# Performance work log

Measured on AMD Instinct MI355X. Metric: run time of the kernel, lower is better.

## Reference

```python
import jax, jax.numpy as jnp
import numpy as np

EPS = 1e-8  # torch.nn.CosineSimilarity default eps


def _cosine_sim(a, b):
    # cosine similarity along channel dim (axis=1), matching torch semantics:
    # dot / (max(||a||, eps) * max(||b||, eps))
    na = jnp.maximum(jnp.sqrt(jnp.sum(a * a, axis=1)), EPS)
    nb = jnp.maximum(jnp.sqrt(jnp.sum(b * b, axis=1)), EPS)
    return jnp.sum(a * b, axis=1) / (na * nb)  # [B, T]


def setup_inputs() -> dict:
    key = jax.random.key(0)
    k1, k2, k3 = jax.random.split(key, 3)
    B, C, T, O, K = 8, 512, 4096, 512, 3
    feature = jax.random.normal(k1, (B, C, T), dtype=jnp.float32)
    embedding = jax.random.normal(k2, (B, C, T), dtype=jnp.float32)
    weight = jax.random.normal(k3, (O, C, K), dtype=jnp.float32) * 0.05
    return {"feature": feature, "embedding": embedding, "weight": weight}


def reference(feature, embedding, weight):
    B, C, T = feature.shape
    O = weight.shape[0]
    K = 3  # kernel_size is structurally 3 in this module

    # shifted embeddings with zero padding (left / right neighbors)
    emb_l = jnp.pad(embedding[:, :, :-1], ((0, 0), (0, 0), (1, 0)))
    emb_r = jnp.pad(embedding[:, :, 1:], ((0, 0), (0, 0), (0, 1)))
    sim = jnp.stack(
        [_cosine_sim(embedding, emb_l),
         _cosine_sim(embedding, embedding),
         _cosine_sim(embedding, emb_r)],
        axis=1,
    )  # [B, 3, T]

    # tile: first C rows = sim_l, next C = sim_c, last C = sim_r -> [B, 3C, T]
    att = jnp.repeat(sim, C, axis=1)

    # im2col (nn.Unfold with kernel (3,1), padding (1,0)): channel-major layout
    f_pad = jnp.pad(feature, ((0, 0), (0, 0), (1, 1)))  # [B, C, T+2]
    inp_unf = jnp.stack([f_pad[:, :, k:k + T] for k in range(K)], axis=2)
    inp_unf = inp_unf.reshape(B, C * K, T)  # row index = c*3 + k (torch unfold order)

    w_flat = weight.reshape(O, C * K)
    # out[b,o,t] = sum_i (inp_unf * att)[b,i,t] * w_flat[o,i]
    out = jnp.einsum('bit,oi->bot', inp_unf * att, w_flat)
    return out
```

## Files before the change

kernel.cpp:

```cpp
#include <hip/hip_runtime.h>
#include <hip/hip_bf16.h>
#include <stdint.h>

#define B_ 8
#define C_ 512
#define T_ 4096
#define O_ 512
#define KP_ 1728
#define EPS_ 1e-8f

#define BM 128
#define BN 128
#define FTP_ROWS 4104

typedef unsigned short ushort_t;
typedef __attribute__((ext_vector_type(4))) float f32x4;
typedef __attribute__((ext_vector_type(8))) short bf16x8;

__device__ __forceinline__ ushort_t f2bf(float f) {
  union { float f; uint32_t u; } x; x.f = f;
  uint32_t u = x.u;
  uint32_t r = (u + 0x7FFFu + ((u >> 16) & 1u)) >> 16;
  return (ushort_t)r;
}

#define GLOAD16(gsrc, ldst) \
  __builtin_amdgcn_global_load_lds((const __attribute__((address_space(1))) unsigned int*)(gsrc), \
                                   (__attribute__((address_space(3))) unsigned int*)(ldst), 16, 0, 0)

__global__ void sim_reduce_kernel(const float* __restrict__ emb,
                                  float* __restrict__ nn_out,
                                  float* __restrict__ dl_out) {
  const int b = blockIdx.y;
  const int t0 = (blockIdx.x * 64 + threadIdx.x) * 4;
  const int cty = threadIdx.y;
  float nn0=0.f,nn1=0.f,nn2=0.f,nn3=0.f;
  float dl0=0.f,dl1=0.f,dl2=0.f,dl3=0.f;
  const float* base = emb + (size_t)b * C_ * T_;
  for (int c = cty * 128; c < cty * 128 + 128; ++c) {
    const float* row = base + (size_t)c * T_;
    float4 v = *(const float4*)(row + t0);
    float el = (t0 > 0) ? row[t0 - 1] : 0.f;
    nn0 += v.x*v.x; nn1 += v.y*v.y; nn2 += v.z*v.z; nn3 += v.w*v.w;
    dl0 += v.x*el;  dl1 += v.y*v.x; dl2 += v.z*v.y; dl3 += v.w*v.z;
  }
  __shared__ float red[4][64*8];
  float* myr = &red[cty][threadIdx.x * 8];
  if (cty != 0) {
    myr[0]=nn0; myr[1]=nn1; myr[2]=nn2; myr[3]=nn3;
    myr[4]=dl0; myr[5]=dl1; myr[6]=dl2; myr[7]=dl3;
  }
  __syncthreads();
  if (cty == 0) {
    for (int q = 1; q < 4; ++q) {
      float* r = &red[q][threadIdx.x * 8];
      nn0+=r[0]; nn1+=r[1]; nn2+=r[2]; nn3+=r[3];
      dl0+=r[4]; dl1+=r[5]; dl2+=r[6]; dl3+=r[7];
    }
    float* nb = nn_out + (size_t)b * T_ + t0;
    float* db = dl_out + (size_t)b * T_ + t0;
    nb[0]=nn0; nb[1]=nn1; nb[2]=nn2; nb[3]=nn3;
    db[0]=dl0; db[1]=dl1; db[2]=dl2; db[3]=dl3;
  }
}

__global__ void prep_small_kernel(const float* __restrict__ nn,
                                  const float* __restrict__ dl,
                                  float* __restrict__ rat,
                                  const float* __restrict__ w,
                                  ushort_t* __restrict__ wbf) {
  const int bid = blockIdx.x;
  if (bid < 128) {
    const int idx = bid * 256 + threadIdx.x;
    const int b = idx >> 12;
    const int t = idx & (T_ - 1);
    const float* nnb = nn + (size_t)b * T_;
    const float* dlb = dl + (size_t)b * T_;
    float nncur = nnb[t];
    float ncur = fmaxf(sqrtf(nncur), EPS_);
    float sc = nncur / (ncur * ncur);
    float sl = 0.f, sr = 0.f;
    if (t > 0) {
      float np = fmaxf(sqrtf(nnb[t - 1]), EPS_);
      sl = dlb[t] / (ncur * np);
    }
    if (t < T_ - 1) {
      float nx = fmaxf(sqrtf(nnb[t + 1]), EPS_);
      sr = dlb[t + 1] / (ncur * nx);
    }
    float shr = (fabsf(sr) < 1e-6f) ? copysignf(1e-6f, sr) : sr;
    float shc = fmaxf(sc, 1e-6f);
    float* ratb = rat + (size_t)b * T_;
    ratb[t] = sl / shr;
    ratb[(size_t)B_ * T_ + t] = shr / shc;
    ratb[(size_t)2 * B_ * T_ + t] = sc;
  } else {
    const int idx = (bid - 128) * 256 + threadIdx.x;
    if (idx >= O_ * KP_) return;
    const int o = idx / KP_;
    const int p = idx - o * KP_;
    const int g = p / 576; const int r = p - g * 576;
    const int k = r / 192; const int j = r - k * 192;
    const int c_lo = (512 * g - k + 2) / 3;
    const int c_hi = (512 * g + 511 - k) / 3;
    const int c = (c_lo & ~7) + j;
    float v = (c >= c_lo && c <= c_hi) ? w[((size_t)o * C_ + c) * 3 + k] : 0.f;
    wbf[idx] = f2bf(v);
  }
}

__global__ void transpose_kernel(const float* __restrict__ feat, ushort_t* __restrict__ Ftp) {
  const int b = blockIdx.z;
  const int c0 = blockIdx.y * 64;
  const int tid = threadIdx.x;
  if (blockIdx.x == T_ / 64) {
    if (tid < 64)        Ftp[((size_t)b * FTP_ROWS + 0) * 512 + c0 + tid] = 0;
    else if (tid < 128)  Ftp[((size_t)b * FTP_ROWS + T_ + 1) * 512 + c0 + (tid - 64)] = 0;
    return;
  }
  const int t0 = blockIdx.x * 64;
  __shared__ ushort_t LT[64 * 72];
  {
    const int cl = tid >> 2;
    const int tq = (tid & 3) * 16;
    const float* src = feat + ((size_t)b * C_ + c0 + cl) * T_ + t0 + tq;
    for (int q = 0; q < 4; ++q) {
      float4 v = *(const float4*)(src + q * 4);
      const int t = tq + q * 4;
      LT[(t + 0) * 72 + cl] = f2bf(v.x);
      LT[(t + 1) * 72 + cl] = f2bf(v.y);
      LT[(t + 2) * 72 + cl] = f2bf(v.z);
      LT[(t + 3) * 72 + cl] = f2bf(v.w);
    }
  }
  __syncthreads();
  {
    const int tl = tid >> 2;
    const int cq = (tid & 3) * 16;
    ushort_t* dst = Ftp + ((size_t)b * FTP_ROWS + t0 + tl + 1) * 512 + c0 + cq;
    *(uint4*)(dst) = *(const uint4*)&LT[tl * 72 + cq];
    *(uint4*)(dst + 8) = *(const uint4*)&LT[tl * 72 + cq + 8];
  }
}

__global__ __launch_bounds__(256, 3)
void conv_gemm_kernel(const ushort_t* __restrict__ Ftp,
                      const ushort_t* __restrict__ wbf,
                      const float* __restrict__ rat,
                      float* __restrict__ out) {
  __shared__ __align__(16) ushort_t Al[BM * 64];
  __shared__ __align__(16) ushort_t Bl[BN * 64];

  const int b = blockIdx.z;
  const int oBase = blockIdx.y * BM;
  const int tBase = blockIdx.x * BN;

  const int tid = threadIdx.x;
  const int lane = tid & 63;
  const int wid = tid >> 6;
  const int wm = wid >> 1;
  const int wn = wid & 1;
  const int llo = lane & 15, lhi = lane >> 4;

  const int r8 = lane >> 3;
  const int chs = ((lane & 7) ^ r8) * 8;

  const ushort_t* aS = wbf + (size_t)(oBase + wid * 32 + r8) * KP_ + chs;
  const ushort_t* bS = Ftp + ((size_t)b * FTP_ROWS + tBase + wid * 32 + r8) * 512 + chs;

  ushort_t* aD = &Al[(wid * 32) * 64 + lane * 8];
  ushort_t* bD = &Bl[(wid * 32) * 64 + lane * 8];

  const int fra = (wm * 64 + llo) * 64 + ((lhi ^ (llo & 7)) * 8);
  const int frb = (wn * 64 + llo) * 64 + ((lhi ^ (llo & 7)) * 8);

  const float* ratB = rat + (size_t)b * T_ + tBase + wn * 64 + llo;

  f32x4 acc[4][4];
  const f32x4 vzero = {0.f, 0.f, 0.f, 0.f};
#pragma unroll
  for (int m = 0; m < 4; ++m)
#pragma unroll
    for (int n = 0; n < 4; ++n) acc[m][n] = vzero;

#pragma unroll
  for (int u = 0; u < 27; ++u) {
    const int s2 = (u < 9) ? u : ((u < 18) ? u + 9 : u - 9);
    const int g = s2 / 9, rr = s2 - g * 9, k = rr / 3, jb = rr - k * 3;
    const int c_st = ((512 * g - k + 2) / 3) & ~7;
    const int boff = k * 512 + c_st + jb * 64;

    __syncthreads();
#pragma unroll
    for (int i = 0; i < 4; ++i) {
      GLOAD16(aS + (size_t)(i * 8) * KP_ + s2 * 64, aD + i * 512);
      GLOAD16(bS + (size_t)(i * 8) * 512 + boff,    bD + i * 512);
    }
    __syncthreads();

#pragma unroll
    for (int h = 0; h < 2; ++h) {
      bf16x8 af[4], bfv[4];
#pragma unroll
      for (int m = 0; m < 4; ++m)
        af[m] = *(const bf16x8*)&Al[(fra ^ (h * 32)) + m * 1024];
#pragma unroll
      for (int n = 0; n < 4; ++n)
        bfv[n] = *(const bf16x8*)&Bl[(frb ^ (h * 32)) + n * 1024];
#pragma unroll
      for (int m = 0; m < 4; ++m)
#pragma unroll
        for (int n = 0; n < 4; ++n)
          acc[m][n] = __builtin_amdgcn_mfma_f32_16x16x32_bf16(af[m], bfv[n], acc[m][n], 0, 0, 0);
    }

    if (u == 8 || u == 17 || u == 26) {
      const int sel = (u == 8) ? 0 : (u == 17) ? 1 : 2;
#pragma unroll
      for (int n = 0; n < 4; ++n) {
        const float s = ratB[(size_t)sel * B_ * T_ + n * 16];
#pragma unroll
        for (int m = 0; m < 4; ++m) acc[m][n] *= s;
      }
    }
  }

  float* outB = out + ((size_t)b * O_ + oBase) * T_ + tBase;
#pragma unroll
  for (int m = 0; m < 4; ++m) {
    const int r0 = wm * 64 + m * 16 + lhi * 4;
#pragma unroll
    for (int n = 0; n < 4; ++n) {
      const int cg = wn * 64 + n * 16 + llo;
#pragma unroll
      for (int r = 0; r < 4; ++r)
        outB[(size_t)(r0 + r) * T_ + cg] = acc[m][n][r];
    }
  }
}

extern "C" void kernel_launch(void* const* d_in, const int* in_sizes, int n_in,
                              void* d_out, int out_size, void* d_ws, size_t ws_size,
                              hipStream_t stream) {
  const float* feature   = (const float*)d_in[0];
  const float* embedding = (const float*)d_in[1];
  const float* weight    = (const float*)d_in[2];
  float* out = (float*)d_out;

  float* ws  = (float*)d_ws;
  float* nn  = ws;
  float* dl  = nn + (size_t)B_ * T_;
  float* rat = dl + (size_t)B_ * T_;
  ushort_t* wbf = (ushort_t*)(rat + (size_t)3 * B_ * T_);
  ushort_t* Ftp = wbf + (size_t)O_ * KP_;

  sim_reduce_kernel<<<dim3(T_ / 256, B_), dim3(64, 4), 0, stream>>>(embedding, nn, dl);
  prep_small_kernel<<<dim3(128 + (O_ * KP_ + 255) / 256), 256, 0, stream>>>(nn, dl, rat, weight, wbf);
  transpose_kernel<<<dim3(T_ / 64 + 1, C_ / 64, B_), 256, 0, stream>>>(feature, Ftp);
  conv_gemm_kernel<<<dim3(T_ / BN, O_ / BM, B_), 256, 0, stream>>>(Ftp, wbf, rat, out);
}
```

Before: 116.7 us.

## Enlarge GEMM tile to 256x256 with double-buffered LDS pipeline

Moves the conv GEMM from 128x128 tiles with 256 threads to 256x256 tiles with 512 threads (8 waves, each holding 8x4 MFMA accumulators). It double-buffers LDS through dynamic shared memory and issues the next k-step's global-to-LDS loads while the current step's MFMAs run, using vmcnt waits, barriers and setprio. The rat scale factors are now loaded into registers once up front. This targets load latency and per-tile memory traffic, at the cost of higher register and LDS pressure, lower occupancy, and only 256 blocks in the grid.

```diff
diff --git a/kernel.cpp b/kernel.cpp
--- a/kernel.cpp
+++ b/kernel.cpp
@@ -9,9 +9,12 @@
 #define KP_ 1728
 #define EPS_ 1e-8f
 
-#define BM 128
-#define BN 128
+#define BM 256
+#define BN 256
 #define FTP_ROWS 4104
+
+#define BUF_USH 32768
+#define LDS_BYTES (2 * BUF_USH * 2)
 
 typedef unsigned short ushort_t;
 typedef __attribute__((ext_vector_type(4))) float f32x4;
@@ -143,13 +146,12 @@
   }
 }
 
-__global__ __launch_bounds__(256, 3)
+__global__ __launch_bounds__(512, 2)
 void conv_gemm_kernel(const ushort_t* __restrict__ Ftp,
                       const ushort_t* __restrict__ wbf,
                       const float* __restrict__ rat,
                       float* __restrict__ out) {
-  __shared__ __align__(16) ushort_t Al[BM * 64];
-  __shared__ __align__(16) ushort_t Bl[BN * 64];
+  extern __shared__ ushort_t lds[];
 
   const int b = blockIdx.z;
   const int oBase = blockIdx.y * BM;
@@ -158,77 +160,118 @@
   const int tid = threadIdx.x;
   const int lane = tid & 63;
   const int wid = tid >> 6;
-  const int wm = wid >> 1;
-  const int wn = wid & 1;
+  const int wm = wid >> 2;
+  const int wn = wid & 3;
   const int llo = lane & 15, lhi = lane >> 4;
 
-  const int r8 = lane >> 3;
-  const int chs = ((lane & 7) ^ r8) * 8;
-
-  const ushort_t* aS = wbf + (size_t)(oBase + wid * 32 + r8) * KP_ + chs;
-  const ushort_t* bS = Ftp + ((size_t)b * FTP_ROWS + tBase + wid * 32 + r8) * 512 + chs;
-
-  ushort_t* aD = &Al[(wid * 32) * 64 + lane * 8];
-  ushort_t* bD = &Bl[(wid * 32) * 64 + lane * 8];
-
-  const int fra = (wm * 64 + llo) * 64 + ((lhi ^ (llo & 7)) * 8);
-  const int frb = (wn * 64 + llo) * 64 + ((lhi ^ (llo & 7)) * 8);
+  const int rsw = (lhi ^ ((llo >> 1) & 3)) * 8;
+  const int aRdOff = (wm * 128 + llo) * 32 + rsw;
+  const int bRdOff = 16384 + (wn * 64 + llo) * 32 + rsw;
+
+  const int schunk = ((lane & 3) ^ ((lane >> 3) & 3)) * 8;
+  const int srow = wid * 16 + (lane >> 2);
+
+  const ushort_t* ftpB = Ftp + (size_t)b * FTP_ROWS * 512;
 
   const float* ratB = rat + (size_t)b * T_ + tBase + wn * 64 + llo;
-
-  f32x4 acc[4][4];
+  float rv[3][4];
+#pragma unroll
+  for (int g = 0; g < 3; ++g)
+#pragma unroll
+    for (int n = 0; n < 4; ++n) {
+      rv[g][n] = ratB[(size_t)g * B_ * T_ + n * 16];
+      asm volatile("" : "+v"(rv[g][n]));
+    }
+  asm volatile("s_waitcnt vmcnt(0)" ::: "memory");
+
+  f32x4 acc[8][4];
   const f32x4 vzero = {0.f, 0.f, 0.f, 0.f};
 #pragma unroll
-  for (int m = 0; m < 4; ++m)
+  for (int m = 0; m < 8; ++m)
 #pragma unroll
     for (int n = 0; n < 4; ++n) acc[m][n] = vzero;
 
-#pragma unroll
-  for (int u = 0; u < 27; ++u) {
-    const int s2 = (u < 9) ? u : ((u < 18) ? u + 9 : u - 9);
+  auto STAGE_HALF = [&](int t1, int p) {
+    const int s2 = (t1 < 9) ? t1 : (t1 < 18 ? t1 + 9 : t1 - 9);
+    const int h = p >> 1, isB = p & 1;
     const int g = s2 / 9, rr = s2 - g * 9, k = rr / 3, jb = rr - k * 3;
     const int c_st = ((512 * g - k + 2) / 3) & ~7;
-    const int boff = k * 512 + c_st + jb * 64;
-
-    __syncthreads();
-#pragma unroll
-    for (int i = 0; i < 4; ++i) {
-      GLOAD16(aS + (size_t)(i * 8) * KP_ + s2 * 64, aD + i * 512);
-      GLOAD16(bS + (size_t)(i * 8) * 512 + boff,    bD + i * 512);
-    }
-    __syncthreads();
-
-#pragma unroll
-    for (int h = 0; h < 2; ++h) {
-      bf16x8 af[4], bfv[4];
-#pragma unroll
-      for (int m = 0; m < 4; ++m)
-        af[m] = *(const bf16x8*)&Al[(fra ^ (h * 32)) + m * 1024];
-#pragma unroll
-      for (int n = 0; n < 4; ++n)
-        bfv[n] = *(const bf16x8*)&Bl[(frb ^ (h * 32)) + n * 1024];
-#pragma unroll
-      for (int m = 0; m < 4; ++m)
+    ushort_t* d = lds + (t1 & 1) * BUF_USH + isB * 16384 + h * 8192 + wid * 512;
+    if (!isB) {
+      const ushort_t* s = wbf + (size_t)(oBase + srow) * KP_ + s2 * 64 + h * 32 + schunk;
+      GLOAD16(s, d);
+      GLOAD16(s + (size_t)128 * KP_, d + 4096);
+    } else {
+      const ushort_t* s = ftpB + (size_t)(tBase + srow) * 512 + k * 512 + c_st + jb * 64 + h * 32 + schunk;
+      GLOAD16(s, d);
+      GLOAD16(s + (size_t)128 * 512, d + 4096);
+    }
+  };
+
+  STAGE_HALF(0, 0); STAGE_HALF(0, 1); STAGE_HALF(0, 2); STAGE_HALF(0, 3);
+  asm volatile("s_waitcnt vmcnt(0)" ::: "memory");
+  __builtin_amdgcn_s_barrier();
+  asm volatile("" ::: "memory");
+
+  bf16x8 bfv[2][4];
+
+#pragma unroll
+  for (int t = 0; t < 27; ++t) {
+    const uint32_t rb = (uint32_t)(t & 1) * BUF_USH;
+#pragma unroll
+    for (int p = 0; p < 4; ++p) {
+      const int h = p >> 1, mh = p & 1;
+
+      if (mh == 0) {
 #pragma unroll
         for (int n = 0; n < 4; ++n)
-          acc[m][n] = __builtin_amdgcn_mfma_f32_16x16x32_bf16(af[m], bfv[n], acc[m][n], 0, 0, 0);
-    }
-
-    if (u == 8 || u == 17 || u == 26) {
-      const int sel = (u == 8) ? 0 : (u == 17) ? 1 : 2;
-#pragma unroll
-      for (int n = 0; n < 4; ++n) {
-        const float s = ratB[(size_t)sel * B_ * T_ + n * 16];
-#pragma unroll
-        for (int m = 0; m < 4; ++m) acc[m][n] *= s;
+          bfv[h][n] = *(const bf16x8*)&lds[rb + h * 8192 + bRdOff + n * 512];
       }
+      bf16x8 af[4];
+#pragma unroll
+      for (int mm = 0; mm < 4; ++mm)
+        af[mm] = *(const bf16x8*)&lds[rb + h * 8192 + aRdOff + (mh * 4 + mm) * 512];
+
+      if (t + 1 < 27) STAGE_HALF(t + 1, p);
+
+      if (p == 1) {
+        if (t == 26) { asm volatile("s_waitcnt vmcnt(0)" ::: "memory"); }
+        else         { asm volatile("s_waitcnt vmcnt(4)" ::: "memory"); }
+      } else if (p == 3 && t < 26) {
+        asm volatile("s_waitcnt vmcnt(4)" ::: "memory");
+      }
+      __builtin_amdgcn_s_barrier();
+      asm volatile("s_waitcnt lgkmcnt(0)" ::: "memory");
+      __builtin_amdgcn_sched_barrier(0);
+
+      __builtin_amdgcn_s_setprio(1);
+#pragma unroll
+      for (int mm = 0; mm < 4; ++mm)
+#pragma unroll
+        for (int n = 0; n < 4; ++n)
+          acc[mh * 4 + mm][n] =
+              __builtin_amdgcn_mfma_f32_16x16x32_bf16(af[mm], bfv[h][n], acc[mh * 4 + mm][n], 0, 0, 0);
+      __builtin_amdgcn_s_setprio(0);
+
+      if (p == 3 && (t == 8 || t == 17 || t == 26)) {
+        const int sel = (t == 8) ? 0 : (t == 17) ? 1 : 2;
+#pragma unroll
+        for (int n = 0; n < 4; ++n) {
+          const float s = rv[sel][n];
+#pragma unroll
+          for (int m = 0; m < 8; ++m) acc[m][n] *= s;
+        }
+      }
+
+      __builtin_amdgcn_s_barrier();
+      asm volatile("" ::: "memory");
     }
   }
 
   float* outB = out + ((size_t)b * O_ + oBase) * T_ + tBase;
 #pragma unroll
-  for (int m = 0; m < 4; ++m) {
-    const int r0 = wm * 64 + m * 16 + lhi * 4;
+  for (int m = 0; m < 8; ++m) {
+    const int r0 = wm * 128 + m * 16 + lhi * 4;
 #pragma unroll
     for (int n = 0; n < 4; ++n) {
       const int cg = wn * 64 + n * 16 + llo;
@@ -254,8 +297,11 @@
   ushort_t* wbf = (ushort_t*)(rat + (size_t)3 * B_ * T_);
   ushort_t* Ftp = wbf + (size_t)O_ * KP_;
 
+  (void)hipFuncSetAttribute((const void*)conv_gemm_kernel,
+                            hipFuncAttributeMaxDynamicSharedMemorySize, LDS_BYTES);
+
   sim_reduce_kernel<<<dim3(T_ / 256, B_), dim3(64, 4), 0, stream>>>(embedding, nn, dl);
   prep_small_kernel<<<dim3(128 + (O_ * KP_ + 255) / 256), 256, 0, stream>>>(nn, dl, rat, weight, wbf);
   transpose_kernel<<<dim3(T_ / 64 + 1, C_ / 64, B_), 256, 0, stream>>>(feature, Ftp);
-  conv_gemm_kernel<<<dim3(T_ / BN, O_ / BM, B_), 256, 0, stream>>>(Ftp, wbf, rat, out);
-}
+  conv_gemm_kernel<<<dim3(T_ / BN, O_ / BM, B_), 512, LDS_BYTES, stream>>>(Ftp, wbf, rat, out);
+}
```

After: 103.3 us, median of 4. 11.5% less time.
